# Kernel optimization log

Measured on AMD Instinct MI355X. Metric: run time of the kernel, lower is better.

The kernel has to match this reference:

```python
import jax, jax.numpy as jnp
import numpy as np

HIDDEN = 4096
HEADS = 32
HEAD_DIM = HIDDEN // HEADS  # 128; kv length must equal this (additive-bias broadcast)
B, SQ, SK = 4, 2048, HEAD_DIM


def _split_heads(x):
    # [B, T, HIDDEN] -> [B, H, T, d]
    b, t, _ = x.shape
    return x.reshape(b, t, HEADS, HEAD_DIM).transpose(0, 2, 1, 3)


def setup_inputs() -> dict:
    key = jax.random.key(0)
    ks = jax.random.split(key, 8)
    s = 1.0 / np.sqrt(HIDDEN)
    return {
        "q": jax.random.normal(ks[0], (B, SQ, HIDDEN), jnp.float32),
        "k": jax.random.normal(ks[1], (B, SK, HIDDEN), jnp.float32),
        "v": jax.random.normal(ks[2], (B, SK, HIDDEN), jnp.float32),
        "r": jax.random.normal(ks[3], (B, SQ, HIDDEN), jnp.float32),
        "Wq": jax.random.normal(ks[4], (HIDDEN, HIDDEN), jnp.float32) * s,
        "Wk": jax.random.normal(ks[5], (HIDDEN, HIDDEN), jnp.float32) * s,
        "Wv": jax.random.normal(ks[6], (HIDDEN, HIDDEN), jnp.float32) * s,
        "Wo": jax.random.normal(ks[7], (HIDDEN, HIDDEN), jnp.float32) * s,
    }


def reference(q, k, v, r, Wq, Wk, Wv, Wo):
    qh = _split_heads(q @ Wq)           # [B,H,SQ,d]
    kh = _split_heads(k @ Wk)           # [B,H,SK,d]
    vh = _split_heads(v @ Wv)           # [B,H,SK,d]
    rh = _split_heads(r @ Wo)           # [B,H,SQ,d] ; d == SK, added as bias
    scale = 1.0 / np.sqrt(HEAD_DIM).astype(np.float32)
    scores = jnp.einsum("bhqd,bhkd->bhqk", qh, kh) * scale + rh
    attn = jax.nn.softmax(scores, axis=-1)
    ctx = jnp.einsum("bhqk,bhkd->bhqd", attn, vh)       # [B,H,SQ,d]
    ctx = ctx.transpose(0, 2, 1, 3).reshape(q.shape[0], -1, HIDDEN)
    return ctx @ Wo  # Wo reused for output projection, as in source
```

## Files before the change

kernel.cpp:

```cpp
#include <hip/hip_runtime.h>
#include <hip/hip_bf16.h>

typedef unsigned short u16;
typedef unsigned int   u32;
typedef unsigned long long u64;
typedef __attribute__((ext_vector_type(8))) short short8;
typedef __attribute__((ext_vector_type(4))) float f32x4;

#define HID   4096
#define NHEAD 32
#define HD    128
#define NB    4
#define NSQ   2048
#define NSK   128
#define MROWS (NB*NSQ)
#define KROWS (NB*NSK)

__device__ __forceinline__ u16 f2bf(float f) {
  u32 u = __builtin_bit_cast(u32, f);
  u += 0x7fffu + ((u >> 16) & 1u);
  return (u16)(u >> 16);
}

__device__ __forceinline__ float bf2f(u16 x) {
  u32 u = (u32)x << 16;
  return __builtin_bit_cast(float, u);
}

__device__ __forceinline__ u64 pack4(float4 f) {
  return (u64)f2bf(f.x) | ((u64)f2bf(f.y) << 16) |
         ((u64)f2bf(f.z) << 32) | ((u64)f2bf(f.w) << 48);
}

__device__ __forceinline__ uint4 packu16x8(const u16* v) {
  uint4 o;
  o.x = (u32)v[0] | ((u32)v[1] << 16);
  o.y = (u32)v[2] | ((u32)v[3] << 16);
  o.z = (u32)v[4] | ((u32)v[5] << 16);
  o.w = (u32)v[6] | ((u32)v[7] << 16);
  return o;
}

__device__ __forceinline__ f32x4 mfma16(short8 a, short8 b, f32x4 c) {
  return __builtin_amdgcn_mfma_f32_16x16x32_bf16(a, b, c, 0, 0, 0);
}

__device__ __forceinline__ void gload_lds16(const u16* g, u16* l) {
  __builtin_amdgcn_global_load_lds((const __attribute__((address_space(1))) u32*)g,
                                   (__attribute__((address_space(3))) u32*)l, 16, 0, 0);
}

__global__ __launch_bounds__(256) void convert_bf16_x2(const float* __restrict__ in0,
                                                       u16* __restrict__ out0,
                                                       const float* __restrict__ in1,
                                                       u16* __restrict__ out1, long long n4)
{
  const float* in = blockIdx.y ? in1 : in0;
  u16* out = blockIdx.y ? out1 : out0;
  long long i = (long long)blockIdx.x * blockDim.x + threadIdx.x;
  const long long stride = (long long)gridDim.x * blockDim.x;
  for (; i < n4; i += stride) {
    float4 f = ((const float4*)in)[i];
    ((u64*)out)[i] = pack4(f);
  }
}

__global__ __launch_bounds__(256) void transpose_convert_x4(const float* __restrict__ W0, u16* __restrict__ T0,
                                                            const float* __restrict__ W1, u16* __restrict__ T1,
                                                            const float* __restrict__ W2, u16* __restrict__ T2,
                                                            const float* __restrict__ W3, u16* __restrict__ T3)
{
  const int z = blockIdx.z;
  const float* W = (z == 0) ? W0 : (z == 1) ? W1 : (z == 2) ? W2 : W3;
  u16* Wt = (z == 0) ? T0 : (z == 1) ? T1 : (z == 2) ? T2 : T3;
  __shared__ __align__(16) u16 tile[64][72];
  const int t = threadIdx.x;
  const int c0 = blockIdx.x * 64, r0 = blockIdx.y * 64;
  #pragma unroll
  for (int i = 0; i < 4; ++i) {
    int e = i * 1024 + t * 4;
    int rr = e >> 6, cc = e & 63;
    float4 f = *(const float4*)(W + (size_t)(r0 + rr) * HID + c0 + cc);
    *(u64*)&tile[rr][cc] = pack4(f);
  }
  __syncthreads();
  #pragma unroll
  for (int i = 0; i < 2; ++i) {
    int e = i * 2048 + t * 8;
    int cc = e >> 6, rr = e & 63;
    u16 vals[8];
    #pragma unroll
    for (int jj = 0; jj < 8; ++jj) vals[jj] = tile[rr + jj][cc];
    *(uint4*)(Wt + (size_t)(c0 + cc) * HID + r0 + rr) = packu16x8(vals);
  }
}

__global__ __launch_bounds__(256) void transpose_head(const u16* __restrict__ Vh,
                                                      u16* __restrict__ VT)
{
  __shared__ __align__(16) u16 tile[128][136];
  const int t = threadIdx.x;
  const int bh = blockIdx.x;
  const int b = bh >> 5, h = bh & 31;
  #pragma unroll
  for (int i = 0; i < 8; ++i) {
    int e = i * 2048 + t * 8;
    int tr = e >> 7, d = e & 127;
    *(uint4*)&tile[tr][d] = *(const uint4*)(Vh + ((size_t)b * NSK + tr) * HID + h * HD + d);
  }
  __syncthreads();
  #pragma unroll
  for (int i = 0; i < 8; ++i) {
    int e = i * 2048 + t * 8;
    int d = e >> 7, tt = e & 127;
    u16 vals[8];
    #pragma unroll
    for (int jj = 0; jj < 8; ++jj) vals[jj] = tile[tt + jj][d];
    *(uint4*)(VT + ((size_t)bh * HD + d) * NSK + tt) = packu16x8(vals);
  }
}


__device__ __forceinline__ short8 ldf(const u16* buf, int r, int cb) {
  return *(const short8*)(buf + r * 64 + (cb ^ ((r & 7) << 3)));
}

__device__ __forceinline__ void stage2(u16* dst, const u16* g, long off0, long off1, int tid) {
  gload_lds16(g + off0, dst + tid * 8);
  gload_lds16(g + off1, dst + 4096 + tid * 8);
}

template<int VM, bool S1, bool S2>
__device__ __forceinline__ void tile2(const u16* __restrict__ Ag, const u16* __restrict__ Bg,
                                      int kt, u16* Ac, u16* Bc, u16* Ao, u16* Bo,
                                      int wm, int wn, int g, int c16,
                                      long off0, long off1, int tid, f32x4 (&acc)[8][4])
{
  const int g8 = g * 8;
  short8 af[4][2], bf[4][2];

  if constexpr (S1) {
    stage2(Ao + 8192, Ag + (size_t)128 * HID + kt + 64, off0, off1, tid);
    stage2(Bo + 8192, Bg + (size_t)128 * HID + kt + 64, off0, off1, tid);
  }
  #pragma unroll
  for (int i = 0; i < 4; ++i) {
    const int r = wm * 128 + i * 16 + c16;
    af[i][0] = ldf(Ac, r, g8); af[i][1] = ldf(Ac, r, 32 + g8);
  }
  #pragma unroll
  for (int j = 0; j < 4; ++j) {
    const int r = wn * 64 + j * 16 + c16;
    bf[j][0] = ldf(Bc, r, g8); bf[j][1] = ldf(Bc, r, 32 + g8);
  }
  asm volatile("s_waitcnt lgkmcnt(8)" ::: "memory");
  __builtin_amdgcn_s_barrier();
  asm volatile("s_waitcnt lgkmcnt(0)" ::: "memory");
  __builtin_amdgcn_sched_barrier(0);
  __builtin_amdgcn_s_setprio(1);
  #pragma unroll
  for (int i = 0; i < 4; ++i)
    #pragma unroll
    for (int j = 0; j < 4; ++j)
      acc[i][j] = mfma16(af[i][0], bf[j][0], acc[i][j]);
  #pragma unroll
  for (int i = 0; i < 4; ++i)
    #pragma unroll
    for (int j = 0; j < 4; ++j)
      acc[i][j] = mfma16(af[i][1], bf[j][1], acc[i][j]);
  __builtin_amdgcn_s_setprio(0);

  #pragma unroll
  for (int i = 0; i < 4; ++i) {
    const int r = wm * 128 + 64 + i * 16 + c16;
    af[i][0] = ldf(Ac, r, g8); af[i][1] = ldf(Ac, r, 32 + g8);
  }
  if constexpr (S2) {
    stage2(Bc, Bg + kt + 128, off0, off1, tid);
    stage2(Ac, Ag + kt + 128, off0, off1, tid);
  }
  if constexpr (VM == 4) {
    asm volatile("s_waitcnt vmcnt(4)" ::: "memory");
  } else if constexpr (VM == 0) {
    asm volatile("s_waitcnt vmcnt(0)" ::: "memory");
  }
  __builtin_amdgcn_s_barrier();
  asm volatile("s_waitcnt lgkmcnt(0)" ::: "memory");
  __builtin_amdgcn_sched_barrier(0);
  __builtin_amdgcn_s_setprio(1);
  #pragma unroll
  for (int i = 0; i < 4; ++i)
    #pragma unroll
    for (int j = 0; j < 4; ++j)
      acc[4 + i][j] = mfma16(af[i][0], bf[j][0], acc[4 + i][j]);
  #pragma unroll
  for (int i = 0; i < 4; ++i)
    #pragma unroll
    for (int j = 0; j < 4; ++j)
      acc[4 + i][j] = mfma16(af[i][1], bf[j][1], acc[4 + i][j]);
  __builtin_amdgcn_s_setprio(0);
}

template<bool OUTF32>
__device__ __forceinline__ void gemm_body(const u16* __restrict__ Ag,
                                          const u16* __restrict__ Bg,
                                          u16* __restrict__ Ch, float* __restrict__ Cf,
                                          int n0, int tid,
                                          u16* As0, u16* As1, u16* Bs0, u16* Bs1)
{
  const int l = tid & 63, wv = tid >> 6;
  const int g = l >> 4 & 3, c16 = l & 15;
  const int wm = wv >> 2, wn = wv & 3;

  const long off0 = (long)(tid >> 3) * HID + (((tid & 7) ^ ((tid >> 3) & 7)) * 8);
  const long off1 = off0 + (long)64 * HID;

  f32x4 acc[8][4] = {};

  stage2(Bs0,        Bg,                     off0, off1, tid);
  stage2(As0,        Ag,                     off0, off1, tid);
  stage2(As0 + 8192, Ag + (size_t)128 * HID, off0, off1, tid);
  stage2(Bs0 + 8192, Bg + (size_t)128 * HID, off0, off1, tid);
  stage2(Bs1,        Bg + 64,                off0, off1, tid);
  stage2(As1,        Ag + 64,                off0, off1, tid);
  asm volatile("s_waitcnt vmcnt(4)" ::: "memory");
  __builtin_amdgcn_sched_barrier(0);
  __builtin_amdgcn_s_barrier();

  constexpr int NT = HID / 64;
  for (int T = 0; T < NT - 3; T += 2) {
    tile2<4, true, true>(Ag, Bg, T * 64,      As0, Bs0, As1, Bs1,
                         wm, wn, g, c16, off0, off1, tid, acc);
    tile2<4, true, true>(Ag, Bg, T * 64 + 64, As1, Bs1, As0, Bs0,
                         wm, wn, g, c16, off0, off1, tid, acc);
  }
  tile2<0, true, false>(Ag, Bg, (NT - 2) * 64, As0, Bs0, As1, Bs1,
                        wm, wn, g, c16, off0, off1, tid, acc);
  tile2<-1, false, false>(Ag, Bg, (NT - 1) * 64, As1, Bs1, As0, Bs0,
                          wm, wn, g, c16, off0, off1, tid, acc);

  #pragma unroll
  for (int mi = 0; mi < 8; ++mi)
    #pragma unroll
    for (int j = 0; j < 4; ++j)
      #pragma unroll
      for (int rr = 0; rr < 4; ++rr) {
        const size_t idx = (size_t)(wm * 128 + mi * 16 + g * 4 + rr) * HID
                         + n0 + wn * 64 + j * 16 + c16;
        if constexpr (OUTF32) Cf[idx] = acc[mi][j][rr];
        else                  Ch[idx] = f2bf(acc[mi][j][rr]);
      }
}

__global__ __launch_bounds__(512, 2) void gemm_mega(const u16* __restrict__ qb,
                                                    const u16* __restrict__ WqT,
                                                    u16* __restrict__ Qh,
                                                    const u16* __restrict__ rb,
                                                    const u16* __restrict__ WoT,
                                                    u16* __restrict__ Rhb,
                                                    const u16* __restrict__ kvb,
                                                    const u16* __restrict__ WkT,
                                                    const u16* __restrict__ WvT,
                                                    u16* __restrict__ Kh,
                                                    u16* __restrict__ Vh,
                                                    int nQ, int nR)
{
  __shared__ __align__(16) u16 As[2][16384];
  __shared__ __align__(16) u16 Bs[2][16384];
  const int tid = threadIdx.x;

  const int nwg = gridDim.x;
  int wg = blockIdx.x;
  wg = (wg & 7) * (nwg >> 3) + (wg >> 3);

  const u16* Ag; const u16* Bg; u16* Ch; int n0;
  if (wg < nQ) {
    const int m0 = (wg >> 4) * 256; n0 = (wg & 15) * 256;
    Ag = qb + (size_t)m0 * HID;  Bg = WqT + (size_t)n0 * HID;  Ch = Qh + (size_t)m0 * HID;
  } else if (wg < nQ + nR) {
    const int e = wg - nQ;
    const int m0 = (e >> 4) * 256; n0 = (e & 15) * 256;
    Ag = rb + (size_t)m0 * HID;  Bg = WoT + (size_t)n0 * HID;  Ch = Rhb + (size_t)m0 * HID;
  } else {
    const int e = wg - nQ - nR, mt = e >> 4;
    n0 = (e & 15) * 256;
    Ag = kvb + (size_t)(mt << 8) * HID;
    Bg = (mt < 2 ? WkT : WvT) + (size_t)n0 * HID;
    Ch = (mt < 2 ? Kh : Vh) + (size_t)((mt & 1) << 8) * HID;
  }

  gemm_body<false>(Ag, Bg, Ch, nullptr, n0, tid, &As[0][0], &As[1][0], &Bs[0][0], &Bs[1][0]);
}

__global__ __launch_bounds__(512, 2) void gemm256f(const u16* __restrict__ A,
                                                   const u16* __restrict__ Bt,
                                                   float* __restrict__ C)
{
  __shared__ __align__(16) u16 As[2][16384];
  __shared__ __align__(16) u16 Bs[2][16384];
  const int tid = threadIdx.x;

  const int nwg = gridDim.x;
  int wg = blockIdx.x;
  wg = (wg & 7) * (nwg >> 3) + (wg >> 3);
  const int m0 = (wg >> 4) * 256, n0 = (wg & 15) * 256;

  gemm_body<true>(A + (size_t)m0 * HID, Bt + (size_t)n0 * HID,
                  nullptr, C + (size_t)m0 * HID, n0, tid,
                  &As[0][0], &As[1][0], &Bs[0][0], &Bs[1][0]);
}

__global__ __launch_bounds__(256) void attn_kernel(const u16*  __restrict__ Qh,
                                                   const u16*  __restrict__ Kh,
                                                   const u16*  __restrict__ VT,
                                                   const u16*  __restrict__ Rhb,
                                                   u16* __restrict__ ctx)
{
  __shared__ __align__(16) u16 sh[4][32][136];
  const int t = threadIdx.x;
  const int w = t >> 6, l = t & 63;
  const int g = l >> 4, c = l & 15;
  const int qc = blockIdx.x;
  const int bh = blockIdx.y;
  const int b = bh >> 5, h = bh & 31;
  const size_t qrow0 = (size_t)b * NSQ + qc * 128 + w * 32;
  const float SCALE = 0.08838834764831845f;

  const u16* brow = Rhb + ((size_t)b * NSQ + qc * 128) * HID + h * HD;
  #pragma unroll
  for (int it = 0; it < 8; ++it) {
    int e = it * 2048 + t * 8;
    int rr_ = e >> 7, cc = e & 127;
    *(uint4*)&sh[rr_ >> 5][rr_ & 31][cc] = *(const uint4*)(brow + (size_t)rr_ * HID + cc);
  }

  f32x4 s[2][8] = {};
  #pragma unroll
  for (int ks = 0; ks < 4; ++ks) {
    const int ko = ks * 32 + g * 8;
    short8 af[2];
    #pragma unroll
    for (int i = 0; i < 2; ++i)
      af[i] = *(const short8*)(Qh + (qrow0 + i * 16 + c) * HID + h * HD + ko);
    #pragma unroll
    for (int j = 0; j < 8; ++j) {
      short8 bfr = *(const short8*)(Kh + ((size_t)b * NSK + j * 16 + c) * HID + h * HD + ko);
      s[0][j] = mfma16(af[0], bfr, s[0][j]);
      s[1][j] = mfma16(af[1], bfr, s[1][j]);
    }
  }
  __syncthreads();

  float rinv[2][4];
  #pragma unroll
  for (int i = 0; i < 2; ++i) {
    #pragma unroll
    for (int rr = 0; rr < 4; ++rr) {
      const int lr = i * 16 + g * 4 + rr;
      float vmax = -3.0e38f;
      #pragma unroll
      for (int j = 0; j < 8; ++j) {
        float bias = bf2f(sh[w][lr][j * 16 + c]);
        float sv = s[i][j][rr] * SCALE + bias;
        s[i][j][rr] = sv;
        vmax = fmaxf(vmax, sv);
      }
      #pragma unroll
      for (int m = 1; m < 16; m <<= 1) vmax = fmaxf(vmax, __shfl_xor(vmax, m));
      float ssum = 0.f;
      #pragma unroll
      for (int j = 0; j < 8; ++j) {
        float p = __expf(s[i][j][rr] - vmax);
        s[i][j][rr] = p;
        ssum += p;
      }
      #pragma unroll
      for (int m = 1; m < 16; m <<= 1) ssum += __shfl_xor(ssum, m);
      rinv[i][rr] = 1.f / ssum;
    }
  }

  #pragma unroll
  for (int i = 0; i < 2; ++i)
    #pragma unroll
    for (int j = 0; j < 8; ++j)
      #pragma unroll
      for (int rr = 0; rr < 4; ++rr)
        sh[w][i * 16 + g * 4 + rr][j * 16 + c] = f2bf(s[i][j][rr]);
  __syncthreads();

  #pragma unroll
  for (int i = 0; i < 2; ++i) {
    f32x4 o[8] = {};
    #pragma unroll
    for (int ks = 0; ks < 4; ++ks) {
      const int ko = ks * 32 + g * 8;
      short8 pa = *(const short8*)(&sh[w][i * 16 + c][ko]);
      #pragma unroll
      for (int j = 0; j < 8; ++j) {
        short8 bv = *(const short8*)(VT + ((size_t)bh * HD + j * 16 + c) * NSK + ko);
        o[j] = mfma16(pa, bv, o[j]);
      }
    }
    #pragma unroll
    for (int j = 0; j < 8; ++j)
      #pragma unroll
      for (int rr = 0; rr < 4; ++rr) {
        const size_t row = qrow0 + i * 16 + g * 4 + rr;
        ctx[row * HID + h * HD + j * 16 + c] = f2bf(o[j][rr] * rinv[i][rr]);
      }
  }
}

extern "C" void kernel_launch(void* const* d_in, const int* in_sizes, int n_in,
                              void* d_out, int out_size, void* d_ws, size_t ws_size,
                              hipStream_t stream)
{
  const float* q  = (const float*)d_in[0];
  const float* k  = (const float*)d_in[1];
  const float* v  = (const float*)d_in[2];
  const float* r  = (const float*)d_in[3];
  const float* Wq = (const float*)d_in[4];
  const float* Wk = (const float*)d_in[5];
  const float* Wv = (const float*)d_in[6];
  const float* Wo = (const float*)d_in[7];
  float* out = (float*)d_out;

  char* ws = (char*)d_ws;
  #define WSMB(x) ((size_t)(x) << 20)
  u16* WoT = (u16*)(ws + WSMB(0));
  u16* Qh  = (u16*)(ws + WSMB(32));
  u16* Kh  = (u16*)(ws + WSMB(96));
  u16* Vh  = (u16*)(ws + WSMB(100));
  u16* VTb = (u16*)(ws + WSMB(104));
  u16* rb  = (u16*)(ws + WSMB(108));
  u16* ctx = (u16*)(ws + WSMB(108));
  u16* Sb  = (u16*)(ws + WSMB(172));
  u16* WqT = (u16*)(ws + WSMB(236));
  u16* WkT = (u16*)((char*)d_out + WSMB(0));
  u16* WvT = (u16*)((char*)d_out + WSMB(32));
  u16* kvb = (u16*)((char*)d_out + WSMB(64));
  u16* vbp = kvb + (size_t)KROWS * HID;
  const size_t needed = WSMB(268);
  if (ws_size < needed) return;

  dim3 tb(256);
  dim3 tb5(512);
  const long long nBig = (long long)MROWS * HID / 4;
  const long long nSm  = (long long)KROWS * HID / 4;

  transpose_convert_x4<<<dim3(64, 64, 4), tb, 0, stream>>>(Wo, WoT, Wq, WqT, Wk, WkT, Wv, WvT);
  convert_bf16_x2<<<dim3(512, 2), tb, 0, stream>>>(k, kvb, v, vbp, nSm);
  convert_bf16_x2<<<dim3(2048, 2), tb, 0, stream>>>(q, Sb, r, rb, nBig);

  gemm_mega<<<dim3(576), tb5, 0, stream>>>(Sb, WqT, Qh, nullptr, nullptr, nullptr,
                                           kvb, WkT, WvT, Kh, Vh, 512, 0);
  gemm_mega<<<dim3(512), tb5, 0, stream>>>(nullptr, nullptr, nullptr, rb, WoT, Sb,
                                           nullptr, nullptr, nullptr, nullptr, nullptr, 0, 512);

  transpose_head<<<dim3(128), tb, 0, stream>>>(Vh, VTb);

  attn_kernel<<<dim3(16, 128), tb, 0, stream>>>(Qh, Kh, VTb, Sb, ctx);

  gemm256f<<<dim3(512), tb5, 0, stream>>>(ctx, WoT, out);
}
```

Measured before the change: 1.150 ms.

## Software-pipeline LDS fragment loads across MFMA phases in GEMM tile loop

Restructures the GEMM inner tile so that A-fragment loads for the second half and for the next tile are issued between MFMA groups, with extra register arrays (ah) holding prefetched fragments. The first A fragments are preloaded before the loop. This hides LDS read latency behind matrix instructions. In exchange it raises register pressure, which could cause spills under 512-thread, 2-block launch bounds. It also adds a correctness risk from reading the other buffer before its barrier.

```diff
diff --git a/kernel.cpp b/kernel.cpp
--- a/kernel.cpp
+++ b/kernel.cpp
@@ -130,30 +130,25 @@
   gload_lds16(g + off1, dst + 4096 + tid * 8);
 }
 
-template<int VM, bool S1, bool S2>
+template<int VM, bool S1, bool S2, bool NEXT>
 __device__ __forceinline__ void tile2(const u16* __restrict__ Ag, const u16* __restrict__ Bg,
                                       int kt, u16* Ac, u16* Bc, u16* Ao, u16* Bo,
                                       int wm, int wn, int g, int c16,
-                                      long off0, long off1, int tid, f32x4 (&acc)[8][4])
+                                      long off0, long off1, int tid,
+                                      short8 (&af)[4][2], short8 (&ah)[4][2],
+                                      short8 (&bf)[4][2], f32x4 (&acc)[8][4])
 {
   const int g8 = g * 8;
-  short8 af[4][2], bf[4][2];
-
+
+  #pragma unroll
+  for (int j = 0; j < 4; ++j) {
+    const int r = wn * 64 + j * 16 + c16;
+    bf[j][0] = ldf(Bc, r, g8); bf[j][1] = ldf(Bc, r, 32 + g8);
+  }
   if constexpr (S1) {
     stage2(Ao + 8192, Ag + (size_t)128 * HID + kt + 64, off0, off1, tid);
     stage2(Bo + 8192, Bg + (size_t)128 * HID + kt + 64, off0, off1, tid);
   }
-  #pragma unroll
-  for (int i = 0; i < 4; ++i) {
-    const int r = wm * 128 + i * 16 + c16;
-    af[i][0] = ldf(Ac, r, g8); af[i][1] = ldf(Ac, r, 32 + g8);
-  }
-  #pragma unroll
-  for (int j = 0; j < 4; ++j) {
-    const int r = wn * 64 + j * 16 + c16;
-    bf[j][0] = ldf(Bc, r, g8); bf[j][1] = ldf(Bc, r, 32 + g8);
-  }
-  asm volatile("s_waitcnt lgkmcnt(8)" ::: "memory");
   __builtin_amdgcn_s_barrier();
   asm volatile("s_waitcnt lgkmcnt(0)" ::: "memory");
   __builtin_amdgcn_sched_barrier(0);
@@ -163,6 +158,15 @@
     #pragma unroll
     for (int j = 0; j < 4; ++j)
       acc[i][j] = mfma16(af[i][0], bf[j][0], acc[i][j]);
+  __builtin_amdgcn_s_setprio(0);
+  __builtin_amdgcn_sched_barrier(0);
+  #pragma unroll
+  for (int i = 0; i < 4; ++i) {
+    const int r = wm * 128 + 64 + i * 16 + c16;
+    ah[i][0] = ldf(Ac, r, g8); ah[i][1] = ldf(Ac, r, 32 + g8);
+  }
+  __builtin_amdgcn_sched_barrier(0);
+  __builtin_amdgcn_s_setprio(1);
   #pragma unroll
   for (int i = 0; i < 4; ++i)
     #pragma unroll
@@ -170,11 +174,6 @@
       acc[i][j] = mfma16(af[i][1], bf[j][1], acc[i][j]);
   __builtin_amdgcn_s_setprio(0);
 
-  #pragma unroll
-  for (int i = 0; i < 4; ++i) {
-    const int r = wm * 128 + 64 + i * 16 + c16;
-    af[i][0] = ldf(Ac, r, g8); af[i][1] = ldf(Ac, r, 32 + g8);
-  }
   if constexpr (S2) {
     stage2(Bc, Bg + kt + 128, off0, off1, tid);
     stage2(Ac, Ag + kt + 128, off0, off1, tid);
@@ -192,12 +191,23 @@
   for (int i = 0; i < 4; ++i)
     #pragma unroll
     for (int j = 0; j < 4; ++j)
-      acc[4 + i][j] = mfma16(af[i][0], bf[j][0], acc[4 + i][j]);
+      acc[4 + i][j] = mfma16(ah[i][0], bf[j][0], acc[4 + i][j]);
+  __builtin_amdgcn_s_setprio(0);
+  __builtin_amdgcn_sched_barrier(0);
+  if constexpr (NEXT) {
+    #pragma unroll
+    for (int i = 0; i < 4; ++i) {
+      const int r = wm * 128 + i * 16 + c16;
+      af[i][0] = ldf(Ao, r, g8); af[i][1] = ldf(Ao, r, 32 + g8);
+    }
+  }
+  __builtin_amdgcn_sched_barrier(0);
+  __builtin_amdgcn_s_setprio(1);
   #pragma unroll
   for (int i = 0; i < 4; ++i)
     #pragma unroll
     for (int j = 0; j < 4; ++j)
-      acc[4 + i][j] = mfma16(af[i][1], bf[j][1], acc[4 + i][j]);
+      acc[4 + i][j] = mfma16(ah[i][1], bf[j][1], acc[4 + i][j]);
   __builtin_amdgcn_s_setprio(0);
 }
 
@@ -211,11 +221,13 @@
   const int l = tid & 63, wv = tid >> 6;
   const int g = l >> 4 & 3, c16 = l & 15;
   const int wm = wv >> 2, wn = wv & 3;
+  const int g8 = g * 8;
 
   const long off0 = (long)(tid >> 3) * HID + (((tid & 7) ^ ((tid >> 3) & 7)) * 8);
   const long off1 = off0 + (long)64 * HID;
 
   f32x4 acc[8][4] = {};
+  short8 af[4][2], ah[4][2], bf[4][2];
 
   stage2(Bs0,        Bg,                     off0, off1, tid);
   stage2(As0,        Ag,                     off0, off1, tid);
@@ -226,18 +238,23 @@
   asm volatile("s_waitcnt vmcnt(4)" ::: "memory");
   __builtin_amdgcn_sched_barrier(0);
   __builtin_amdgcn_s_barrier();
+  #pragma unroll
+  for (int i = 0; i < 4; ++i) {
+    const int r = wm * 128 + i * 16 + c16;
+    af[i][0] = ldf(As0, r, g8); af[i][1] = ldf(As0, r, 32 + g8);
+  }
 
   constexpr int NT = HID / 64;
   for (int T = 0; T < NT - 3; T += 2) {
-    tile2<4, true, true>(Ag, Bg, T * 64,      As0, Bs0, As1, Bs1,
-                         wm, wn, g, c16, off0, off1, tid, acc);
-    tile2<4, true, true>(Ag, Bg, T * 64 + 64, As1, Bs1, As0, Bs0,
-                         wm, wn, g, c16, off0, off1, tid, acc);
-  }
-  tile2<0, true, false>(Ag, Bg, (NT - 2) * 64, As0, Bs0, As1, Bs1,
-                        wm, wn, g, c16, off0, off1, tid, acc);
-  tile2<-1, false, false>(Ag, Bg, (NT - 1) * 64, As1, Bs1, As0, Bs0,
-                          wm, wn, g, c16, off0, off1, tid, acc);
+    tile2<4, true, true, true>(Ag, Bg, T * 64,      As0, Bs0, As1, Bs1,
+                               wm, wn, g, c16, off0, off1, tid, af, ah, bf, acc);
+    tile2<4, true, true, true>(Ag, Bg, T * 64 + 64, As1, Bs1, As0, Bs0,
+                               wm, wn, g, c16, off0, off1, tid, af, ah, bf, acc);
+  }
+  tile2<0, true, false, true>(Ag, Bg, (NT - 2) * 64, As0, Bs0, As1, Bs1,
+                              wm, wn, g, c16, off0, off1, tid, af, ah, bf, acc);
+  tile2<-1, false, false, false>(Ag, Bg, (NT - 1) * 64, As1, Bs1, As0, Bs0,
+                                 wm, wn, g, c16, off0, off1, tid, af, ah, bf, acc);
 
   #pragma unroll
   for (int mi = 0; mi < 8; ++mi)
```

Result: faster. 1.047 ms (-8.9%).
